# Optimization experiments

Measured on AMD Instinct MI355X. Metric: run time of the kernel, lower is better.

## Reference

```python
import jax, jax.numpy as jnp
import numpy as np

B, N_STATES, STATE_SIZE = 32768, 16, 32
ENC, HID, OUT = 64, 128, 8


def setup_inputs() -> dict:
    key = jax.random.key(0)
    ks = jax.random.split(key, 8)
    states = jax.random.normal(ks[0], (B, N_STATES, STATE_SIZE), dtype=jnp.float32)
    # validity flags: first element of each per-field state. agent state (index 0)
    # always valid; neighbor states valid with prob 0.7 (contiguity enforced in reference
    # via cumprod, matching the original while-loop semantics).
    flags = (jax.random.uniform(ks[1], (B, N_STATES)) < 0.7).astype(jnp.float32)
    flags = flags.at[:, 0].set(1.0)
    states = states.at[:, :, 0].set(flags)
    obs_flat = states.reshape(B, N_STATES * STATE_SIZE)
    s = 0.05
    return {
        "obs_flat": obs_flat,
        "W_enc": jax.random.normal(ks[2], (STATE_SIZE, ENC), dtype=jnp.float32) * s,
        "b_enc": jnp.zeros((ENC,), dtype=jnp.float32),
        "W_f": jax.random.normal(ks[3], (2 * ENC, HID), dtype=jnp.float32) * s,
        "b_f": jnp.zeros((HID,), dtype=jnp.float32),
        "W_dec": jax.random.normal(ks[4], (HID, OUT), dtype=jnp.float32) * s,
        "b_dec": jnp.zeros((OUT,), dtype=jnp.float32),
    }


def reference(obs_flat, W_enc, b_enc, W_f, b_f, W_dec, b_dec):
    Bsz = obs_flat.shape[0]
    states = obs_flat.reshape(Bsz, N_STATES, STATE_SIZE)          # [B,N,S]
    flags = states[:, :, 0]                                        # [B,N]
    # original: while-loop stops at first invalid state -> contiguous-prefix validity
    neigh_valid = jnp.cumprod((flags[:, 1:] == 1.0).astype(jnp.float32), axis=1)  # [B,N-1]
    enc = jax.nn.relu(jnp.einsum('bns,se->bne', states, W_enc) + b_enc)            # [B,N,E]
    agent_enc = enc[:, 0]                                          # [B,E]
    neigh_enc = enc[:, 1:]                                         # [B,N-1,E]
    cnt = jnp.sum(neigh_valid, axis=1)                             # [B]
    # mean aggregation over valid neighbors; zero vector if none (original aggregates [zeros])
    agg = jnp.einsum('bne,bn->be', neigh_enc, neigh_valid) / jnp.maximum(cnt, 1.0)[:, None]
    f_in = jnp.concatenate([agent_enc, agg], axis=-1)              # [B,2E]
    hidden = jax.nn.relu(f_in @ W_f + b_f)                         # [B,H]
    logits = hidden @ W_dec + b_dec                                # [B,O]
    return logits
```

## Files before the change

### kernel.cpp

```cpp
#include <hip/hip_runtime.h>
#include <stdint.h>

#define NB    32768
#define NS    16
#define SS    32
#define ENCD  64
#define HIDD  128
#define OUTD  8
#define BT    16
#define THREADS 256

typedef _Float16 half8  __attribute__((ext_vector_type(8)));
typedef __fp16   fp16x2 __attribute__((ext_vector_type(2)));
typedef float    f32x4  __attribute__((ext_vector_type(4)));

#define MFMA(a, b, c) __builtin_amdgcn_mfma_f32_16x16x32_f16((a), (b), (c), 0, 0, 0)

__device__ __forceinline__ void split8(const float* f, half8& hi, half8& lo) {
#pragma unroll
  for (int j = 0; j < 8; j += 2) {
    fp16x2 h  = __builtin_amdgcn_cvt_pkrtz(f[j], f[j + 1]);
    float  r0 = f[j]     - (float)h[0];
    float  r1 = f[j + 1] - (float)h[1];
    fp16x2 l2 = __builtin_amdgcn_cvt_pkrtz(r0, r1);
    hi[j] = (_Float16)(float)h[0];  hi[j + 1] = (_Float16)(float)h[1];
    lo[j] = (_Float16)(float)l2[0]; lo[j + 1] = (_Float16)(float)l2[1];
  }
}

__global__ __launch_bounds__(THREADS, 4)
void gnn_fused(const float* __restrict__ obs,
               const float* __restrict__ W_enc,
               const float* __restrict__ b_enc,
               const float* __restrict__ W_f,
               const float* __restrict__ b_f,
               const float* __restrict__ W_dec,
               const float* __restrict__ b_dec,
               float* __restrict__ out)
{
  __shared__ __align__(16) float f_in[BT][132];
  __shared__ __align__(16) float hidn[BT][132];

  const int tid  = threadIdx.x;
  const int w    = tid >> 6;
  const int l    = tid & 63;
  const int m15  = l & 15;
  const int quad = l >> 4;
  const int b0   = blockIdx.x * BT;

  half8 we_hi[4], we_lo[4];
  float benc[4];
#pragma unroll
  for (int nt = 0; nt < 4; ++nt) {
    float f[8];
#pragma unroll
    for (int j = 0; j < 8; ++j)
      f[j] = W_enc[(size_t)(quad * 8 + j) * ENCD + nt * 16 + m15];
    split8(f, we_hi[nt], we_lo[nt]);
    benc[nt] = b_enc[nt * 16 + m15];
  }

  const float* bp = obs + (size_t)(b0 + w * 4) * (NS * SS) + m15 * SS + quad * 8;
  float4 c0 = ((const float4*)bp)[0];
  float4 c1 = ((const float4*)bp)[1];
#pragma unroll
  for (int i = 0; i < 4; ++i) {
    float4 n0, n1;
    if (i < 3) {
      const float* np = bp + (size_t)(i + 1) * (NS * SS);
      n0 = ((const float4*)np)[0];
      n1 = ((const float4*)np)[1];
    } else { n0 = c0; n1 = c1; }

    float f[8] = {c0.x, c0.y, c0.z, c0.w, c1.x, c1.y, c1.z, c1.w};

    unsigned long long bal = __ballot((l < 16) && (f[0] == 1.0f));
    int run = __builtin_ctzll(~(bal >> 1));
    float inv = 1.0f / fmaxf((float)run, 1.0f);

    half8 ahi, alo;
    split8(f, ahi, alo);

    const int bi = w * 4 + i;
#pragma unroll
    for (int nt = 0; nt < 4; ++nt) {
      f32x4 acc = {0.f, 0.f, 0.f, 0.f};
      acc = MFMA(ahi, we_hi[nt], acc);
      acc = MFMA(alo, we_hi[nt], acc);
      acc = MFMA(ahi, we_lo[nt], acc);
      float s = 0.f, e0 = 0.f;
#pragma unroll
      for (int r = 0; r < 4; ++r) {
        int n = quad * 4 + r;
        float v = fmaxf(acc[r] + benc[nt], 0.f);
        if (n == 0) e0 = v;
        if (n >= 1 && n <= run) s += v;
      }
      s += __shfl_xor(s, 16, 64);
      s += __shfl_xor(s, 32, 64);
      if (quad == 0) {
        f_in[bi][nt * 16 + m15]      = e0;
        f_in[bi][64 + nt * 16 + m15] = s * inv;
      }
    }
    c0 = n0; c1 = n1;
  }
  __syncthreads();

  {
    half8 fa_hi[4], fa_lo[4];
#pragma unroll
    for (int ks = 0; ks < 4; ++ks) {
      const float4* p = (const float4*)&f_in[m15][ks * 32 + quad * 8];
      float4 a = p[0], b = p[1];
      float f[8] = {a.x, a.y, a.z, a.w, b.x, b.y, b.z, b.w};
      split8(f, fa_hi[ks], fa_lo[ks]);
    }

#pragma unroll
    for (int tt = 0; tt < 2; ++tt) {
      const int h0 = (w * 2 + tt) * 16 + m15;
      f32x4 acc = {0.f, 0.f, 0.f, 0.f};
#pragma unroll
      for (int ks = 0; ks < 4; ++ks) {
        float f[8];
#pragma unroll
        for (int j = 0; j < 8; ++j)
          f[j] = W_f[(size_t)(ks * 32 + quad * 8 + j) * HIDD + h0];
        half8 bhi, blo;
        split8(f, bhi, blo);
        acc = MFMA(fa_hi[ks], bhi, acc);
        acc = MFMA(fa_lo[ks], bhi, acc);
        acc = MFMA(fa_hi[ks], blo, acc);
      }
      const float bfv = b_f[h0];
#pragma unroll
      for (int r = 0; r < 4; ++r)
        hidn[quad * 4 + r][h0] = fmaxf(acc[r] + bfv, 0.f);
    }
  }
  __syncthreads();

  if (w == 0) {
    half8 ga_hi[4], ga_lo[4];
#pragma unroll
    for (int ks = 0; ks < 4; ++ks) {
      const float4* p = (const float4*)&hidn[m15][ks * 32 + quad * 8];
      float4 a = p[0], b = p[1];
      float f[8] = {a.x, a.y, a.z, a.w, b.x, b.y, b.z, b.w};
      split8(f, ga_hi[ks], ga_lo[ks]);
    }
    f32x4 acc = {0.f, 0.f, 0.f, 0.f};
#pragma unroll
    for (int ks = 0; ks < 4; ++ks) {
      float f[8];
#pragma unroll
      for (int j = 0; j < 8; ++j) {
        int k = ks * 32 + quad * 8 + j;
        f[j] = (m15 < OUTD) ? W_dec[(size_t)k * OUTD + m15] : 0.f;
      }
      half8 bhi, blo;
      split8(f, bhi, blo);
      acc = MFMA(ga_hi[ks], bhi, acc);
      acc = MFMA(ga_lo[ks], bhi, acc);
      acc = MFMA(ga_hi[ks], blo, acc);
    }
    if (m15 < OUTD) {
      const float bd = b_dec[m15];
#pragma unroll
      for (int r = 0; r < 4; ++r) {
        const int m = quad * 4 + r;
        out[(size_t)(b0 + m) * OUTD + m15] = acc[r] + bd;
      }
    }
  }
}

extern "C" void kernel_launch(void* const* d_in, const int* in_sizes, int n_in,
                              void* d_out, int out_size, void* d_ws, size_t ws_size,
                              hipStream_t stream) {
  (void)in_sizes; (void)n_in; (void)d_ws; (void)ws_size; (void)out_size;
  const float* obs   = (const float*)d_in[0];
  const float* W_enc = (const float*)d_in[1];
  const float* b_enc = (const float*)d_in[2];
  const float* W_f   = (const float*)d_in[3];
  const float* b_f   = (const float*)d_in[4];
  const float* W_dec = (const float*)d_in[5];
  const float* b_dec = (const float*)d_in[6];
  float* out = (float*)d_out;

  dim3 grid(NB / BT);
  dim3 block(THREADS);
  gnn_fused<<<grid, block, 0, stream>>>(obs, W_enc, b_enc, W_f, b_f, W_dec, b_dec, out);
}
```

Measured before the change: 113.5 us.

## Give each wave its own 16-row batch tile and drop block barriers

Each wave now handles 16 batch rows end to end: encoder, W_f layer and decoder, using a per-wave LDS scratch that is reused for the layer inputs and the hidden activations. Block-wide __syncthreads calls become per-wave lgkmcnt waits. Each block now covers 64 rows, and the obs loads use a 3-deep register prefetch ring. The aim is to remove barrier stalls and idle waves in the decoder stage. The cost is that each wave computes all 8 hidden tiles, so every wave rereads and resplits the whole of W_f. Register pressure is also higher, and launch bounds drop to 2 blocks per CU.

Result: slower. 116.8 us (+2.9%).

```diff
diff --git a/kernel.cpp b/kernel.cpp
--- a/kernel.cpp
+++ b/kernel.cpp
@@ -7,7 +7,8 @@
 #define ENCD  64
 #define HIDD  128
 #define OUTD  8
-#define BT    16
+#define BPW   16
+#define BT    64
 #define THREADS 256
 
 typedef _Float16 half8  __attribute__((ext_vector_type(8)));
@@ -15,6 +16,7 @@
 typedef float    f32x4  __attribute__((ext_vector_type(4)));
 
 #define MFMA(a, b, c) __builtin_amdgcn_mfma_f32_16x16x32_f16((a), (b), (c), 0, 0, 0)
+#define WAVE_LGKM0() asm volatile("s_waitcnt lgkmcnt(0)" ::: "memory")
 
 __device__ __forceinline__ void split8(const float* f, half8& hi, half8& lo) {
 #pragma unroll
@@ -28,7 +30,7 @@
   }
 }
 
-__global__ __launch_bounds__(THREADS, 4)
+__global__ __launch_bounds__(THREADS, 2)
 void gnn_fused(const float* __restrict__ obs,
                const float* __restrict__ W_enc,
                const float* __restrict__ b_enc,
@@ -38,15 +40,15 @@
                const float* __restrict__ b_dec,
                float* __restrict__ out)
 {
-  __shared__ __align__(16) float f_in[BT][132];
-  __shared__ __align__(16) float hidn[BT][132];
+  __shared__ __align__(16) float scr[4][BPW][132];
 
   const int tid  = threadIdx.x;
   const int w    = tid >> 6;
   const int l    = tid & 63;
   const int m15  = l & 15;
   const int quad = l >> 4;
-  const int b0   = blockIdx.x * BT;
+  const int b0   = blockIdx.x * BT + w * BPW;
+  float (*S)[132] = scr[w];
 
   half8 we_hi[4], we_lo[4];
   float benc[4];
@@ -60,19 +62,23 @@
     benc[nt] = b_enc[nt * 16 + m15];
   }
 
-  const float* bp = obs + (size_t)(b0 + w * 4) * (NS * SS) + m15 * SS + quad * 8;
-  float4 c0 = ((const float4*)bp)[0];
-  float4 c1 = ((const float4*)bp)[1];
+  const float* bp = obs + (size_t)b0 * (NS * SS) + m15 * SS + quad * 8;
+  float4 A0[3], A1[3];
 #pragma unroll
-  for (int i = 0; i < 4; ++i) {
-    float4 n0, n1;
-    if (i < 3) {
-      const float* np = bp + (size_t)(i + 1) * (NS * SS);
-      n0 = ((const float4*)np)[0];
-      n1 = ((const float4*)np)[1];
-    } else { n0 = c0; n1 = c1; }
+  for (int i = 0; i < 3; ++i) {
+    const float4* p = (const float4*)(bp + (size_t)i * (NS * SS));
+    A0[i] = p[0]; A1[i] = p[1];
+  }
 
-    float f[8] = {c0.x, c0.y, c0.z, c0.w, c1.x, c1.y, c1.z, c1.w};
+#pragma unroll
+  for (int i = 0; i < BPW; ++i) {
+    const int sl = i % 3;
+    float f[8] = {A0[sl].x, A0[sl].y, A0[sl].z, A0[sl].w,
+                  A1[sl].x, A1[sl].y, A1[sl].z, A1[sl].w};
+    if (i < BPW - 3) {
+      const float4* p = (const float4*)(bp + (size_t)(i + 3) * (NS * SS));
+      A0[sl] = p[0]; A1[sl] = p[1];
+    }
 
     unsigned long long bal = __ballot((l < 16) && (f[0] == 1.0f));
     int run = __builtin_ctzll(~(bal >> 1));
@@ -81,7 +87,6 @@
     half8 ahi, alo;
     split8(f, ahi, alo);
 
-    const int bi = w * 4 + i;
 #pragma unroll
     for (int nt = 0; nt < 4; ++nt) {
       f32x4 acc = {0.f, 0.f, 0.f, 0.f};
@@ -99,53 +104,51 @@
       s += __shfl_xor(s, 16, 64);
       s += __shfl_xor(s, 32, 64);
       if (quad == 0) {
-        f_in[bi][nt * 16 + m15]      = e0;
-        f_in[bi][64 + nt * 16 + m15] = s * inv;
+        S[i][nt * 16 + m15]      = e0;
+        S[i][64 + nt * 16 + m15] = s * inv;
       }
     }
-    c0 = n0; c1 = n1;
   }
-  __syncthreads();
+  WAVE_LGKM0();
+
+  half8 fa_hi[4], fa_lo[4];
+#pragma unroll
+  for (int ks = 0; ks < 4; ++ks) {
+    const float4* p = (const float4*)&S[m15][ks * 32 + quad * 8];
+    float4 a = p[0], b = p[1];
+    float f[8] = {a.x, a.y, a.z, a.w, b.x, b.y, b.z, b.w};
+    split8(f, fa_hi[ks], fa_lo[ks]);
+  }
+  WAVE_LGKM0();
+
+#pragma unroll 2
+  for (int tt = 0; tt < 8; ++tt) {
+    const int h0 = tt * 16 + m15;
+    f32x4 acc = {0.f, 0.f, 0.f, 0.f};
+#pragma unroll
+    for (int ks = 0; ks < 4; ++ks) {
+      float f[8];
+#pragma unroll
+      for (int j = 0; j < 8; ++j)
+        f[j] = W_f[(size_t)(ks * 32 + quad * 8 + j) * HIDD + h0];
+      half8 bhi, blo;
+      split8(f, bhi, blo);
+      acc = MFMA(fa_hi[ks], bhi, acc);
+      acc = MFMA(fa_lo[ks], bhi, acc);
+      acc = MFMA(fa_hi[ks], blo, acc);
+    }
+    const float bfv = b_f[h0];
+#pragma unroll
+    for (int r = 0; r < 4; ++r)
+      S[quad * 4 + r][h0] = fmaxf(acc[r] + bfv, 0.f);
+  }
+  WAVE_LGKM0();
 
   {
-    half8 fa_hi[4], fa_lo[4];
-#pragma unroll
-    for (int ks = 0; ks < 4; ++ks) {
-      const float4* p = (const float4*)&f_in[m15][ks * 32 + quad * 8];
-      float4 a = p[0], b = p[1];
-      float f[8] = {a.x, a.y, a.z, a.w, b.x, b.y, b.z, b.w};
-      split8(f, fa_hi[ks], fa_lo[ks]);
-    }
-
-#pragma unroll
-    for (int tt = 0; tt < 2; ++tt) {
-      const int h0 = (w * 2 + tt) * 16 + m15;
-      f32x4 acc = {0.f, 0.f, 0.f, 0.f};
-#pragma unroll
-      for (int ks = 0; ks < 4; ++ks) {
-        float f[8];
-#pragma unroll
-        for (int j = 0; j < 8; ++j)
-          f[j] = W_f[(size_t)(ks * 32 + quad * 8 + j) * HIDD + h0];
-        half8 bhi, blo;
-        split8(f, bhi, blo);
-        acc = MFMA(fa_hi[ks], bhi, acc);
-        acc = MFMA(fa_lo[ks], bhi, acc);
-        acc = MFMA(fa_hi[ks], blo, acc);
-      }
-      const float bfv = b_f[h0];
-#pragma unroll
-      for (int r = 0; r < 4; ++r)
-        hidn[quad * 4 + r][h0] = fmaxf(acc[r] + bfv, 0.f);
-    }
-  }
-  __syncthreads();
-
-  if (w == 0) {
     half8 ga_hi[4], ga_lo[4];
 #pragma unroll
     for (int ks = 0; ks < 4; ++ks) {
-      const float4* p = (const float4*)&hidn[m15][ks * 32 + quad * 8];
+      const float4* p = (const float4*)&S[m15][ks * 32 + quad * 8];
       float4 a = p[0], b = p[1];
       float f[8] = {a.x, a.y, a.z, a.w, b.x, b.y, b.z, b.w};
       split8(f, ga_hi[ks], ga_lo[ks]);
```

## Drop weight low-part split and pipeline W_f loads across two output tiles

Applied to the files above, without the earlier changes.

Weights for the encoder and fusion layers now become a single fp16 value instead of a hi/lo pair, which removes one of the three MFMAs per product. The fusion layer computes both of a wave's hidden tiles at once, interleaves their MFMAs, and prefetches the next k-slice of W_f while the current one is used. This cuts MFMA count and exposed load latency. In exchange, weight rounding error now goes straight into the results, which may hurt accuracy, and the extra live registers could raise register pressure.

New measurement: 110.5 us, median of 2. 1.03x faster.

```diff
diff --git a/kernel.cpp b/kernel.cpp
--- a/kernel.cpp
+++ b/kernel.cpp
@@ -26,6 +26,12 @@
     hi[j] = (_Float16)(float)h[0];  hi[j + 1] = (_Float16)(float)h[1];
     lo[j] = (_Float16)(float)l2[0]; lo[j + 1] = (_Float16)(float)l2[1];
   }
+}
+
+__device__ __forceinline__ void cvt8(const float* f, half8& hi) {
+#pragma unroll
+  for (int j = 0; j < 8; ++j)
+    hi[j] = (_Float16)f[j];
 }
 
 __global__ __launch_bounds__(THREADS, 4)
@@ -48,7 +54,7 @@
   const int quad = l >> 4;
   const int b0   = blockIdx.x * BT;
 
-  half8 we_hi[4], we_lo[4];
+  half8 we_hi[4];
   float benc[4];
 #pragma unroll
   for (int nt = 0; nt < 4; ++nt) {
@@ -56,7 +62,7 @@
 #pragma unroll
     for (int j = 0; j < 8; ++j)
       f[j] = W_enc[(size_t)(quad * 8 + j) * ENCD + nt * 16 + m15];
-    split8(f, we_hi[nt], we_lo[nt]);
+    cvt8(f, we_hi[nt]);
     benc[nt] = b_enc[nt * 16 + m15];
   }
 
@@ -87,7 +93,6 @@
       f32x4 acc = {0.f, 0.f, 0.f, 0.f};
       acc = MFMA(ahi, we_hi[nt], acc);
       acc = MFMA(alo, we_hi[nt], acc);
-      acc = MFMA(ahi, we_lo[nt], acc);
       float s = 0.f, e0 = 0.f;
 #pragma unroll
       for (int r = 0; r < 4; ++r) {
@@ -116,27 +121,44 @@
       float f[8] = {a.x, a.y, a.z, a.w, b.x, b.y, b.z, b.w};
       split8(f, fa_hi[ks], fa_lo[ks]);
     }
-
-#pragma unroll
-    for (int tt = 0; tt < 2; ++tt) {
-      const int h0 = (w * 2 + tt) * 16 + m15;
-      f32x4 acc = {0.f, 0.f, 0.f, 0.f};
-#pragma unroll
-      for (int ks = 0; ks < 4; ++ks) {
-        float f[8];
-#pragma unroll
-        for (int j = 0; j < 8; ++j)
-          f[j] = W_f[(size_t)(ks * 32 + quad * 8 + j) * HIDD + h0];
-        half8 bhi, blo;
-        split8(f, bhi, blo);
-        acc = MFMA(fa_hi[ks], bhi, acc);
-        acc = MFMA(fa_lo[ks], bhi, acc);
-        acc = MFMA(fa_hi[ks], blo, acc);
-      }
-      const float bfv = b_f[h0];
-#pragma unroll
-      for (int r = 0; r < 4; ++r)
-        hidn[quad * 4 + r][h0] = fmaxf(acc[r] + bfv, 0.f);
+    const int   h0  = (w * 2) * 16 + m15;
+    const int   h1  = (w * 2 + 1) * 16 + m15;
+    const float bf0 = b_f[h0];
+    const float bf1 = b_f[h1];
+
+    float cur0[8], cur1[8], nxt0[8], nxt1[8];
+#pragma unroll
+    for (int j = 0; j < 8; ++j) {
+      cur0[j] = W_f[(size_t)(quad * 8 + j) * HIDD + h0];
+      cur1[j] = W_f[(size_t)(quad * 8 + j) * HIDD + h1];
+    }
+
+    f32x4 acc0 = {0.f, 0.f, 0.f, 0.f};
+    f32x4 acc1 = {0.f, 0.f, 0.f, 0.f};
+#pragma unroll
+    for (int ks = 0; ks < 4; ++ks) {
+      if (ks < 3) {
+#pragma unroll
+        for (int j = 0; j < 8; ++j) {
+          const size_t row = (size_t)((ks + 1) * 32 + quad * 8 + j) * HIDD;
+          nxt0[j] = W_f[row + h0];
+          nxt1[j] = W_f[row + h1];
+        }
+      }
+      half8 b0h, b1h;
+      cvt8(cur0, b0h);
+      cvt8(cur1, b1h);
+      acc0 = MFMA(fa_hi[ks], b0h, acc0);
+      acc1 = MFMA(fa_hi[ks], b1h, acc1);
+      acc0 = MFMA(fa_lo[ks], b0h, acc0);
+      acc1 = MFMA(fa_lo[ks], b1h, acc1);
+#pragma unroll
+      for (int j = 0; j < 8; ++j) { cur0[j] = nxt0[j]; cur1[j] = nxt1[j]; }
+    }
+#pragma unroll
+    for (int r = 0; r < 4; ++r) {
+      hidn[quad * 4 + r][h0] = fmaxf(acc0[r] + bf0, 0.f);
+      hidn[quad * 4 + r][h1] = fmaxf(acc1[r] + bf1, 0.f);
     }
   }
   __syncthreads();
```
